# Optimization experiments

Hardware: AMD Instinct MI355X
Metric: run time of the kernel (lower is better)

Reference implementation:

```python
import jax, jax.numpy as jnp
import numpy as np

B, OUT, IN, G = 256, 256, 256, 8


def setup_inputs() -> dict:
    key = jax.random.key(0)
    k1, k2, k3, k4 = jax.random.split(key, 4)
    x = jax.random.normal(k1, (B, IN), dtype=jnp.float32)
    # xavier-like scale for spline_weight
    spline_weight = jax.random.normal(k2, (OUT, IN, G), dtype=jnp.float32) * 0.06
    # scaler initialized to ones in torch; use positive values near 1 to exercise the exp
    spline_scaler = jax.random.uniform(k3, (OUT, IN), dtype=jnp.float32, minval=0.5, maxval=1.5)
    # base_activation initialized to zeros in torch; small random to exercise the residual path
    base_activation = jax.random.normal(k4, (OUT, IN), dtype=jnp.float32) * 0.02
    grid = jnp.linspace(-2.0, 2.0, G, dtype=jnp.float32)
    return {
        "x": x,
        "spline_weight": spline_weight,
        "spline_scaler": spline_scaler,
        "base_activation": base_activation,
        "grid": grid,
    }


def reference(x, spline_weight, spline_scaler, base_activation, grid):
    # x: (B, IN) -> out: (B, OUT)
    xn = jnp.tanh(x)                                        # (B, IN)
    # RBF-like basis: exp(-|tanh(x) - grid| * scaler), shape (B, OUT, IN, G)
    dist = jnp.abs(xn[:, None, :, None] - grid[None, None, None, :])  # (B, 1, IN, G)
    basis = jnp.exp(-dist * spline_scaler[None, :, :, None])          # (B, OUT, IN, G)
    # reduce over grid dim with the spline weights
    spline_out = jnp.einsum('boig,oig->boi', basis, spline_weight)    # (B, OUT, IN)
    out = spline_out + base_activation[None, :, :] * xn[:, None, :]   # (B, OUT, IN)
    return jnp.sum(out, axis=-1)                                      # (B, OUT)
```

## Files before the change

### kernel.cpp

```cpp
#include <hip/hip_runtime.h>


#define B_   256
#define OUT_ 256
#define IN_  256
#define G_   8
#define NK   5
#define BG   32
#define ICH  16
#define NIC  (IN_/ICH)
#define OT   64

__global__ __launch_bounds__(256) void kan_prep(
        const float* __restrict__ x,
        const float* __restrict__ w,
        const float* __restrict__ sc,
        const float* __restrict__ ba,
        const float* __restrict__ grid,
        float2* __restrict__ xnk,
        float2* __restrict__ sbt,
        float2* __restrict__ T)
{
    float g[G_];
#pragma unroll
    for (int j = 0; j < G_; ++j) g[j] = grid[j];

    {
        const int idx = blockIdx.x * 256 + threadIdx.x;
        const float xn = tanhf(x[idx]);
        int k = 0;
#pragma unroll
        for (int j = 0; j < G_; ++j) k += (g[j] <= xn) ? 1 : 0;
        k = min(max(k, 2), 6) - 2;
        xnk[idx] = make_float2(xn, (float)k);
    }

    {
        const int i = blockIdx.x;
        const int o = threadIdx.x;
        const int base = o * IN_ + i;
        const float s  = sc[base];
        const float bv = ba[base];

        float Ep[G_], Em[G_];
#pragma unroll
        for (int j = 0; j < G_; ++j) {
            const float wv = w[base * G_ + j];
            const float t  = s * g[j];
            Ep[j] = wv * __expf(t);
            Em[j] = wv * __expf(-t);
        }
#pragma unroll
        for (int kk = 0; kk < NK; ++kk) {
            const int k = kk + 2;
            float A = 0.f, Bv = 0.f;
#pragma unroll
            for (int j = 0; j < G_; ++j) {
                if (j < k) A += Ep[j]; else Bv += Em[j];
            }
            T[(kk * IN_ + i) * OUT_ + o] = make_float2(A, Bv);
        }
        sbt[i * OUT_ + o] = make_float2(s * 1.44269504088896340736f, bv);
    }
}

__global__ __launch_bounds__(256, 2) void kan_main(
        const float2* __restrict__ xnk,
        const float2* __restrict__ sbt,
        const float2* __restrict__ T,
        float* __restrict__ partial)
{
    const int lane = threadIdx.x & 63;
    const int w    = threadIdx.x >> 6;
    const int slab = blockIdx.x & 63;
    const int bg   = blockIdx.x >> 6;
    const int ot   = slab & 3;
    const int ic   = slab >> 2;
    const int o0   = ot * OT;
    const int i0   = ic * ICH;
    const int b0   = bg * BG;

    __shared__ float2 sT[NK * ICH * OT];
    __shared__ float2 sSB[ICH * OT];
    __shared__ float2 sXK[BG * ICH];

    for (int idx = threadIdx.x; idx < NK * ICH * OT; idx += 256) {
        const int kk = idx >> 10;
        const int rem = idx & 1023;
        const int ii = rem >> 6, ol = rem & 63;
        sT[idx] = T[(kk * IN_ + i0 + ii) * OUT_ + o0 + ol];
    }
    for (int idx = threadIdx.x; idx < ICH * OT; idx += 256) {
        const int ii = idx >> 6, ol = idx & 63;
        sSB[idx] = sbt[(i0 + ii) * OUT_ + o0 + ol];
    }
    for (int idx = threadIdx.x; idx < BG * ICH; idx += 256) {
        const int bb = idx >> 4, ii = idx & 15;
        const float2 v = xnk[(b0 + bb) * IN_ + i0 + ii];
        sXK[idx] = make_float2(v.x, __int_as_float(((int)v.y) << 10));
    }
    __syncthreads();

    float acc[8];
#pragma unroll
    for (int bb = 0; bb < 8; ++bb) acc[bb] = 0.f;

    const int wb = w * 8;
    for (int ii = 0; ii < ICH; ++ii) {
        const float2 sb = sSB[ii * OT + lane];
        const int il = ii * OT + lane;
#pragma unroll
        for (int bb = 0; bb < 8; ++bb) {
            const float2 xk = sXK[(wb + bb) * ICH + ii];
            const float2 rec = sT[__float_as_int(xk.y) + il];
            const float t = sb.x * xk.x;
            float a = fmaf(sb.y, xk.x, acc[bb]);
            a       = fmaf(exp2f(-t), rec.x, a);
            acc[bb] = fmaf(exp2f(t),  rec.y, a);
        }
    }

    float* p = partial + ((size_t)ic * B_ + b0 + wb) * OUT_ + o0 + lane;
#pragma unroll
    for (int bb = 0; bb < 8; ++bb) p[bb * OUT_] = acc[bb];
}

__global__ __launch_bounds__(256) void kan_reduce(
        const float* __restrict__ partial, float* __restrict__ out)
{
    const int idx = blockIdx.x * 256 + threadIdx.x;
    float s = 0.f;
#pragma unroll
    for (int c = 0; c < NIC; ++c) s += partial[c * (B_ * OUT_) + idx];
    out[idx] = s;
}

extern "C" void kernel_launch(void* const* d_in, const int* in_sizes, int n_in,
                              void* d_out, int out_size, void* d_ws, size_t ws_size,
                              hipStream_t stream)
{
    const float* x    = (const float*)d_in[0];
    const float* w    = (const float*)d_in[1];
    const float* sc   = (const float*)d_in[2];
    const float* ba   = (const float*)d_in[3];
    const float* grid = (const float*)d_in[4];
    float* out = (float*)d_out;

    char* ws = (char*)d_ws;
    float2* xnk = (float2*)(ws);
    float2* sbt = (float2*)(ws + 512 * 1024);
    float2* T   = (float2*)(ws + 1024 * 1024);
    float*  partial = (float*)(ws + 1024 * 1024 + (size_t)NK * IN_ * OUT_ * sizeof(float2));

    kan_prep<<<IN_, 256, 0, stream>>>(x, w, sc, ba, grid, xnk, sbt, T);
    kan_main<<<64 * (B_ / BG), 256, 0, stream>>>(xnk, sbt, T, partial);
    kan_reduce<<<(B_ * OUT_) / 256, 256, 0, stream>>>(partial, out);
}
```

Before: 86.82 us.

## Fuse prep, main and reduce kernels into one cooperative kernel

Merges the three launches into a single cooperative kernel of 512 blocks, using grid-wide syncs between the prep, main and reduce phases. The prep work is split across all blocks: the first 256 compute tanh and bin indices, the rest build the T tables. The goal is to remove launch gaps and kernel boundary overhead. In exchange it adds two grid barriers and requires all 512 blocks to be co-resident.

```diff
diff --git a/kernel.cpp b/kernel.cpp
--- a/kernel.cpp
+++ b/kernel.cpp
@@ -1,4 +1,7 @@
 #include <hip/hip_runtime.h>
+#include <hip/hip_cooperative_groups.h>
+
+namespace cg = cooperative_groups;
 
 
 #define B_   256
@@ -11,128 +14,132 @@
 #define NIC  (IN_/ICH)
 #define OT   64
 
-__global__ __launch_bounds__(256) void kan_prep(
+__global__ __launch_bounds__(256, 2) void kan_fused(
         const float* __restrict__ x,
         const float* __restrict__ w,
         const float* __restrict__ sc,
         const float* __restrict__ ba,
-        const float* __restrict__ grid,
+        const float* __restrict__ grd,
         float2* __restrict__ xnk,
         float2* __restrict__ sbt,
-        float2* __restrict__ T)
+        float2* __restrict__ T,
+        float*  __restrict__ partial,
+        float*  __restrict__ out)
 {
-    float g[G_];
-#pragma unroll
-    for (int j = 0; j < G_; ++j) g[j] = grid[j];
-
-    {
-        const int idx = blockIdx.x * 256 + threadIdx.x;
-        const float xn = tanhf(x[idx]);
-        int k = 0;
-#pragma unroll
-        for (int j = 0; j < G_; ++j) k += (g[j] <= xn) ? 1 : 0;
-        k = min(max(k, 2), 6) - 2;
-        xnk[idx] = make_float2(xn, (float)k);
-    }
-
-    {
-        const int i = blockIdx.x;
-        const int o = threadIdx.x;
-        const int base = o * IN_ + i;
-        const float s  = sc[base];
-        const float bv = ba[base];
-
-        float Ep[G_], Em[G_];
-#pragma unroll
-        for (int j = 0; j < G_; ++j) {
-            const float wv = w[base * G_ + j];
-            const float t  = s * g[j];
-            Ep[j] = wv * __expf(t);
-            Em[j] = wv * __expf(-t);
-        }
-#pragma unroll
-        for (int kk = 0; kk < NK; ++kk) {
-            const int k = kk + 2;
-            float A = 0.f, Bv = 0.f;
-#pragma unroll
-            for (int j = 0; j < G_; ++j) {
-                if (j < k) A += Ep[j]; else Bv += Em[j];
-            }
-            T[(kk * IN_ + i) * OUT_ + o] = make_float2(A, Bv);
-        }
-        sbt[i * OUT_ + o] = make_float2(s * 1.44269504088896340736f, bv);
-    }
-}
-
-__global__ __launch_bounds__(256, 2) void kan_main(
-        const float2* __restrict__ xnk,
-        const float2* __restrict__ sbt,
-        const float2* __restrict__ T,
-        float* __restrict__ partial)
-{
-    const int lane = threadIdx.x & 63;
-    const int w    = threadIdx.x >> 6;
-    const int slab = blockIdx.x & 63;
-    const int bg   = blockIdx.x >> 6;
-    const int ot   = slab & 3;
-    const int ic   = slab >> 2;
-    const int o0   = ot * OT;
-    const int i0   = ic * ICH;
-    const int b0   = bg * BG;
+    cg::grid_group gg = cg::this_grid();
+    const int blk = blockIdx.x;
 
     __shared__ float2 sT[NK * ICH * OT];
     __shared__ float2 sSB[ICH * OT];
     __shared__ float2 sXK[BG * ICH];
 
-    for (int idx = threadIdx.x; idx < NK * ICH * OT; idx += 256) {
-        const int kk = idx >> 10;
-        const int rem = idx & 1023;
-        const int ii = rem >> 6, ol = rem & 63;
-        sT[idx] = T[(kk * IN_ + i0 + ii) * OUT_ + o0 + ol];
-    }
-    for (int idx = threadIdx.x; idx < ICH * OT; idx += 256) {
-        const int ii = idx >> 6, ol = idx & 63;
-        sSB[idx] = sbt[(i0 + ii) * OUT_ + o0 + ol];
-    }
-    for (int idx = threadIdx.x; idx < BG * ICH; idx += 256) {
-        const int bb = idx >> 4, ii = idx & 15;
-        const float2 v = xnk[(b0 + bb) * IN_ + i0 + ii];
-        sXK[idx] = make_float2(v.x, __int_as_float(((int)v.y) << 10));
-    }
-    __syncthreads();
+    {
+        float g[G_];
+#pragma unroll
+        for (int j = 0; j < G_; ++j) g[j] = grd[j];
 
-    float acc[8];
+        if (blk < 256) {
+            const int idx = blk * 256 + threadIdx.x;
+            const float xn = tanhf(x[idx]);
+            int k = 0;
 #pragma unroll
-    for (int bb = 0; bb < 8; ++bb) acc[bb] = 0.f;
+            for (int j = 0; j < G_; ++j) k += (g[j] <= xn) ? 1 : 0;
+            k = min(max(k, 2), 6) - 2;
+            xnk[idx] = make_float2(xn, (float)k);
+        } else {
+            const int i = blk - 256;
+            const int o = threadIdx.x;
+            const int base = o * IN_ + i;
+            const float s  = sc[base];
+            const float bv = ba[base];
 
-    const int wb = w * 8;
-    for (int ii = 0; ii < ICH; ++ii) {
-        const float2 sb = sSB[ii * OT + lane];
-        const int il = ii * OT + lane;
+            float Ep[G_], Em[G_];
 #pragma unroll
-        for (int bb = 0; bb < 8; ++bb) {
-            const float2 xk = sXK[(wb + bb) * ICH + ii];
-            const float2 rec = sT[__float_as_int(xk.y) + il];
-            const float t = sb.x * xk.x;
-            float a = fmaf(sb.y, xk.x, acc[bb]);
-            a       = fmaf(exp2f(-t), rec.x, a);
-            acc[bb] = fmaf(exp2f(t),  rec.y, a);
+            for (int j = 0; j < G_; ++j) {
+                const float wv = w[base * G_ + j];
+                const float t  = s * g[j];
+                Ep[j] = wv * __expf(t);
+                Em[j] = wv * __expf(-t);
+            }
+#pragma unroll
+            for (int kk = 0; kk < NK; ++kk) {
+                const int k = kk + 2;
+                float A = 0.f, Bv = 0.f;
+#pragma unroll
+                for (int j = 0; j < G_; ++j) {
+                    if (j < k) A += Ep[j]; else Bv += Em[j];
+                }
+                T[(kk * IN_ + i) * OUT_ + o] = make_float2(A, Bv);
+            }
+            sbt[i * OUT_ + o] = make_float2(s * 1.44269504088896340736f, bv);
         }
     }
 
-    float* p = partial + ((size_t)ic * B_ + b0 + wb) * OUT_ + o0 + lane;
+    __threadfence();
+    gg.sync();
+
+    {
+        const int lane = threadIdx.x & 63;
+        const int wv   = threadIdx.x >> 6;
+        const int slab = blk & 63;
+        const int bg   = blk >> 6;
+        const int ot   = slab & 3;
+        const int ic   = slab >> 2;
+        const int o0   = ot * OT;
+        const int i0   = ic * ICH;
+        const int b0   = bg * BG;
+
+        for (int idx = threadIdx.x; idx < NK * ICH * OT; idx += 256) {
+            const int kk = idx >> 10;
+            const int rem = idx & 1023;
+            const int ii = rem >> 6, ol = rem & 63;
+            sT[idx] = T[(kk * IN_ + i0 + ii) * OUT_ + o0 + ol];
+        }
+        for (int idx = threadIdx.x; idx < ICH * OT; idx += 256) {
+            const int ii = idx >> 6, ol = idx & 63;
+            sSB[idx] = sbt[(i0 + ii) * OUT_ + o0 + ol];
+        }
+        for (int idx = threadIdx.x; idx < BG * ICH; idx += 256) {
+            const int bb = idx >> 4, ii = idx & 15;
+            const float2 v = xnk[(b0 + bb) * IN_ + i0 + ii];
+            sXK[idx] = make_float2(v.x, __int_as_float(((int)v.y) << 10));
+        }
+        __syncthreads();
+
+        float acc[8];
 #pragma unroll
-    for (int bb = 0; bb < 8; ++bb) p[bb * OUT_] = acc[bb];
-}
+        for (int bb = 0; bb < 8; ++bb) acc[bb] = 0.f;
 
-__global__ __launch_bounds__(256) void kan_reduce(
-        const float* __restrict__ partial, float* __restrict__ out)
-{
-    const int idx = blockIdx.x * 256 + threadIdx.x;
-    float s = 0.f;
+        const int wb = wv * 8;
+        for (int ii = 0; ii < ICH; ++ii) {
+            const float2 sb = sSB[ii * OT + lane];
+            const int il = ii * OT + lane;
 #pragma unroll
-    for (int c = 0; c < NIC; ++c) s += partial[c * (B_ * OUT_) + idx];
-    out[idx] = s;
+            for (int bb = 0; bb < 8; ++bb) {
+                const float2 xk = sXK[(wb + bb) * ICH + ii];
+                const float2 rec = sT[__float_as_int(xk.y) + il];
+                const float t = sb.x * xk.x;
+                float a = fmaf(sb.y, xk.x, acc[bb]);
+                a       = fmaf(exp2f(-t), rec.x, a);
+                acc[bb] = fmaf(exp2f(t),  rec.y, a);
+            }
+        }
+
+        float* p = partial + ((size_t)ic * B_ + b0 + wb) * OUT_ + o0 + lane;
+#pragma unroll
+        for (int bb = 0; bb < 8; ++bb) p[bb * OUT_] = acc[bb];
+    }
+
+    __threadfence();
+    gg.sync();
+
+    if (blk < 256) {
+        const int idx = blk * 256 + threadIdx.x;
+        float s = 0.f;
+#pragma unroll
+        for (int c = 0; c < NIC; ++c) s += partial[c * (B_ * OUT_) + idx];
+        out[idx] = s;
+    }
 }
 
 extern "C" void kernel_launch(void* const* d_in, const int* in_sizes, int n_in,
@@ -143,7 +150,7 @@
     const float* w    = (const float*)d_in[1];
     const float* sc   = (const float*)d_in[2];
     const float* ba   = (const float*)d_in[3];
-    const float* grid = (const float*)d_in[4];
+    const float* grd  = (const float*)d_in[4];
     float* out = (float*)d_out;
 
     char* ws = (char*)d_ws;
@@ -152,7 +159,9 @@
     float2* T   = (float2*)(ws + 1024 * 1024);
     float*  partial = (float*)(ws + 1024 * 1024 + (size_t)NK * IN_ * OUT_ * sizeof(float2));
 
-    kan_prep<<<IN_, 256, 0, stream>>>(x, w, sc, ba, grid, xnk, sbt, T);
-    kan_main<<<64 * (B_ / BG), 256, 0, stream>>>(xnk, sbt, T, partial);
-    kan_reduce<<<(B_ * OUT_) / 256, 256, 0, stream>>>(partial, out);
+    void* args[] = { (void*)&x, (void*)&w, (void*)&sc, (void*)&ba, (void*)&grd,
+                     (void*)&xnk, (void*)&sbt, (void*)&T, (void*)&partial,
+                     (void*)&out };
+    hipLaunchCooperativeKernel((void*)kan_fused, dim3(512), dim3(256),
+                               args, 0, stream);
 }
```

Measured after the change: 285.8 us. +229.1%, slower.
